# Kernel tuning notes

Measured on AMD Instinct MI355X. Metric: run time of the kernel, lower is better.

Reference implementation:

```python
import jax, jax.numpy as jnp
import numpy as np

B, S, E, H = 2, 2048, 1024, 16
D = E // H  # head dim = 64


def setup_inputs() -> dict:
    key = jax.random.key(0)
    ks = jax.random.split(key, 8)
    s = 1.0 / np.sqrt(E)  # keep projections well-scaled
    return {
        "query": jax.random.normal(ks[0], (B, S, E), jnp.float32),
        "key": jax.random.normal(ks[1], (B, S, E), jnp.float32),
        "value": jax.random.normal(ks[2], (B, S, E), jnp.float32),
        "Wq": jax.random.normal(ks[3], (E, E), jnp.float32) * s,
        "bq": jnp.zeros((E,), jnp.float32),
        "Wk": jax.random.normal(ks[4], (E, E), jnp.float32) * s,
        "bk": jnp.zeros((E,), jnp.float32),
        "Wv": jax.random.normal(ks[5], (E, E), jnp.float32) * s,
        "bv": jnp.zeros((E,), jnp.float32),
        "Wo": jax.random.normal(ks[6], (E, E), jnp.float32) * s,
        "bo": jnp.zeros((E,), jnp.float32),
    }


def _split_heads(x):
    # (b, s, h*d) -> (b, h, s, d)
    b, s, _ = x.shape
    return x.reshape(b, s, H, D).transpose(0, 2, 1, 3)


def reference(query, key, value, Wq, bq, Wk, bk, Wv, bv, Wo, bo):
    # Linear projections (torch Linear: x @ W^T + b)
    q = _split_heads(query @ Wq.T + bq)  # (b, h, s_q, d)
    k = _split_heads(key @ Wk.T + bk)    # (b, h, s_k, d)
    v = _split_heads(value @ Wv.T + bv)  # (b, h, s_k, d)
    # scaled dot-product attention; scale uses head dim of key
    scores = jnp.einsum("bhqd,bhkd->bhqk", q, k) * (D ** -0.5)
    attn = jax.nn.softmax(scores, axis=-1)  # (b, h, s_q, s_k)
    ctx = jnp.einsum("bhqk,bhkd->bhqd", attn, v)
    # merge heads: (b, h, s, d) -> (b, s, h*d)
    ctx = ctx.transpose(0, 2, 1, 3).reshape(B, S, H * D)
    out = ctx @ Wo.T + bo  # (b, s, out_dim)
    return out, attn
```

## Files before the change

kernel.cpp:

```cpp
#include <hip/hip_runtime.h>

typedef _Float16 f16;
typedef _Float16 f16x4 __attribute__((ext_vector_type(4)));
typedef _Float16 f16x8 __attribute__((ext_vector_type(8)));
typedef float f32x4 __attribute__((ext_vector_type(4)));

#define S_LEN 2048
#define EMB 1024
#define NH 16
#define HD 64
#define BATCH 2

__device__ __forceinline__ void gload_lds16(const void* g, void* l) {
  __builtin_amdgcn_global_load_lds(
      (const __attribute__((address_space(1))) void*)g,
      (__attribute__((address_space(3))) void*)l, 16, 0, 0);
}

__global__ __launch_bounds__(256) void cast_kernel(const float* __restrict__ in,
                                                   f16* __restrict__ out, int n4) {
  int i = blockIdx.x * 256 + threadIdx.x;
  if (i >= n4) return;
  const float4 v = reinterpret_cast<const float4*>(in)[i];
  f16x4 o;
  o[0] = (f16)v.x; o[1] = (f16)v.y; o[2] = (f16)v.z; o[3] = (f16)v.w;
  reinterpret_cast<f16x4*>(out)[i] = o;
}

template <int MODE>
__global__ __launch_bounds__(256) void gemm_bt(const f16* __restrict__ A,
                                               const f16* __restrict__ Bw,
                                               const float* __restrict__ bias,
                                               void* __restrict__ outp,
                                               int M, int N, int K) {
  __shared__ f16 As[128 * 64];
  __shared__ f16 Bs[64 * 64];
  const int tid = threadIdx.x;
  const int w = tid >> 6, lane = tid & 63;
  const int lg = lane >> 4, l15 = lane & 15;
  const int m0 = blockIdx.y * 128, n0 = blockIdx.x * 64;
  f32x4 acc[2][4] = {};
  for (int k0 = 0; k0 < K; k0 += 64) {
#pragma unroll
    for (int i = 0; i < 4; i++) {
      int c = i * 4 + w, o = c * 64 + lane;
      gload_lds16(A + (size_t)(m0 + (o >> 3)) * K + k0 + ((o & 7) << 3), As + c * 512);
    }
#pragma unroll
    for (int i = 0; i < 2; i++) {
      int c = i * 4 + w, o = c * 64 + lane;
      gload_lds16(Bw + (size_t)(n0 + (o >> 3)) * K + k0 + ((o & 7) << 3), Bs + c * 512);
    }
    __syncthreads();
#pragma unroll
    for (int kk = 0; kk < 2; kk++) {
      f16x8 af[2], bf[4];
#pragma unroll
      for (int mi = 0; mi < 2; mi++)
        af[mi] = *(const f16x8*)&As[(w * 32 + mi * 16 + l15) * 64 + kk * 32 + lg * 8];
#pragma unroll
      for (int ni = 0; ni < 4; ni++)
        bf[ni] = *(const f16x8*)&Bs[(ni * 16 + l15) * 64 + kk * 32 + lg * 8];
#pragma unroll
      for (int mi = 0; mi < 2; mi++)
#pragma unroll
        for (int ni = 0; ni < 4; ni++)
          acc[mi][ni] =
              __builtin_amdgcn_mfma_f32_16x16x32_f16(af[mi], bf[ni], acc[mi][ni], 0, 0, 0);
    }
    __syncthreads();
  }
#pragma unroll
  for (int mi = 0; mi < 2; mi++)
#pragma unroll
    for (int ni = 0; ni < 4; ni++) {
      const int gn = n0 + ni * 16 + l15;
      const float bv = bias[gn];
#pragma unroll
      for (int r = 0; r < 4; r++) {
        const int gm = m0 + w * 32 + mi * 16 + lg * 4 + r;
        const float v = acc[mi][ni][r] + bv;
        if (MODE == 1) {
          ((float*)outp)[(size_t)gm * N + gn] = v;
        } else {
          const int b = gm >> 11, s = gm & 2047;
          const int h = gn >> 6, d = gn & 63;
          ((f16*)outp)[(((size_t)(b * NH + h)) * S_LEN + s) * HD + d] = (f16)v;
        }
      }
    }
}

__global__ __launch_bounds__(256) void attn_kernel(const f16* __restrict__ Qp,
                                                   const f16* __restrict__ Kp,
                                                   const f16* __restrict__ Vp,
                                                   float* __restrict__ attn_out,
                                                   f16* __restrict__ ctx_out) {
  __shared__ f16 Vt[64 * 136];
  __shared__ f16 Ps[4][16 * 136];
  const int tid = threadIdx.x;
  const int w = tid >> 6, lane = tid & 63;
  const int lg = lane >> 4, l15 = lane & 15;
  const int bh = blockIdx.y;
  const int b = bh >> 4, h = bh & 15;
  const int q0 = blockIdx.x * 64;
  const f16* Qbh = Qp + (size_t)bh * S_LEN * HD;
  const f16* Kbh = Kp + (size_t)bh * S_LEN * HD;
  const f16* Vbh = Vp + (size_t)bh * S_LEN * HD;
  const int qrow_base = q0 + w * 16;

  f16x8 qf[2];
#pragma unroll
  for (int kk = 0; kk < 2; kk++)
    qf[kk] = *(const f16x8*)&Qbh[(size_t)(qrow_base + l15) * HD + kk * 32 + lg * 8];

  float m[4], l[4];
#pragma unroll
  for (int r = 0; r < 4; r++) { m[r] = -1e30f; l[r] = 0.f; }

  for (int kt = 0; kt < S_LEN; kt += 128) {
    f32x4 sf[8] = {};
#pragma unroll
    for (int kk = 0; kk < 2; kk++)
#pragma unroll
      for (int nf = 0; nf < 8; nf++) {
        f16x8 kf = *(const f16x8*)&Kbh[(size_t)(kt + nf * 16 + l15) * HD + kk * 32 + lg * 8];
        sf[nf] = __builtin_amdgcn_mfma_f32_16x16x32_f16(qf[kk], kf, sf[nf], 0, 0, 0);
      }
#pragma unroll
    for (int r = 0; r < 4; r++) {
      float pm = sf[0][r];
#pragma unroll
      for (int nf = 1; nf < 8; nf++) pm = fmaxf(pm, sf[nf][r]);
      pm *= 0.125f;
#pragma unroll
      for (int ofs = 1; ofs < 16; ofs <<= 1) pm = fmaxf(pm, __shfl_xor(pm, ofs));
      const float mn = fmaxf(m[r], pm);
      float ps = 0.f;
#pragma unroll
      for (int nf = 0; nf < 8; nf++) ps += __expf(sf[nf][r] * 0.125f - mn);
#pragma unroll
      for (int ofs = 1; ofs < 16; ofs <<= 1) ps += __shfl_xor(ps, ofs);
      l[r] = l[r] * __expf(m[r] - mn) + ps;
      m[r] = mn;
    }
  }
  float invl[4];
#pragma unroll
  for (int r = 0; r < 4; r++) invl[r] = 1.0f / l[r];

  f32x4 cacc[4] = {};
  for (int kt = 0; kt < S_LEN; kt += 128) {
#pragma unroll
    for (int i = 0; i < 4; i++) {
      int ch = i * 256 + tid;
      int ky = ch >> 3, d0 = (ch & 7) << 3;
      f16x8 v = *(const f16x8*)&Vbh[(size_t)(kt + ky) * HD + d0];
#pragma unroll
      for (int j = 0; j < 8; j++) Vt[(d0 + j) * 136 + ky] = v[j];
    }
    __syncthreads();

    f32x4 sf[8] = {};
#pragma unroll
    for (int kk = 0; kk < 2; kk++)
#pragma unroll
      for (int nf = 0; nf < 8; nf++) {
        f16x8 kf = *(const f16x8*)&Kbh[(size_t)(kt + nf * 16 + l15) * HD + kk * 32 + lg * 8];
        sf[nf] = __builtin_amdgcn_mfma_f32_16x16x32_f16(qf[kk], kf, sf[nf], 0, 0, 0);
      }
#pragma unroll
    for (int nf = 0; nf < 8; nf++)
#pragma unroll
      for (int r = 0; r < 4; r++) {
        const float p = __expf(sf[nf][r] * 0.125f - m[r]) * invl[r];
        const int qrow = qrow_base + lg * 4 + r;
        attn_out[((size_t)bh * S_LEN + qrow) * S_LEN + kt + nf * 16 + l15] = p;
        Ps[w][(lg * 4 + r) * 136 + nf * 16 + l15] = (f16)p;
      }
#pragma unroll
    for (int kk2 = 0; kk2 < 4; kk2++) {
      f16x8 pf = *(const f16x8*)&Ps[w][l15 * 136 + kk2 * 32 + lg * 8];
#pragma unroll
      for (int nf2 = 0; nf2 < 4; nf2++) {
        f16x8 vf = *(const f16x8*)&Vt[(nf2 * 16 + l15) * 136 + kk2 * 32 + lg * 8];
        cacc[nf2] = __builtin_amdgcn_mfma_f32_16x16x32_f16(pf, vf, cacc[nf2], 0, 0, 0);
      }
    }
    __syncthreads();
  }
#pragma unroll
  for (int nf2 = 0; nf2 < 4; nf2++)
#pragma unroll
    for (int r = 0; r < 4; r++) {
      const int qrow = qrow_base + lg * 4 + r;
      const int gr = b * S_LEN + qrow;
      const int gc = h * HD + nf2 * 16 + l15;
      ctx_out[(size_t)gr * EMB + gc] = (f16)cacc[nf2][r];
    }
}

extern "C" void kernel_launch(void* const* d_in, const int* in_sizes, int n_in,
                              void* d_out, int out_size, void* d_ws, size_t ws_size,
                              hipStream_t stream) {
  const float* query = (const float*)d_in[0];
  const float* key_i = (const float*)d_in[1];
  const float* value = (const float*)d_in[2];
  const float* Wq = (const float*)d_in[3];
  const float* bq = (const float*)d_in[4];
  const float* Wk = (const float*)d_in[5];
  const float* bk = (const float*)d_in[6];
  const float* Wv = (const float*)d_in[7];
  const float* bv = (const float*)d_in[8];
  const float* Wo = (const float*)d_in[9];
  const float* bo = (const float*)d_in[10];

  float* out = (float*)d_out;
  float* attn = out + (size_t)BATCH * S_LEN * EMB;

  f16* ws = (f16*)d_ws;
  const size_t NTOK = (size_t)BATCH * S_LEN;
  f16* Qh = ws;
  f16* Kh = Qh + NTOK * EMB;
  f16* Vh = Kh + NTOK * EMB;
  f16* Wqh = Vh + NTOK * EMB;
  f16* Wkh = Wqh + (size_t)EMB * EMB;
  f16* Wvh = Wkh + (size_t)EMB * EMB;
  f16* Woh = Wvh + (size_t)EMB * EMB;
  f16* Qp = Woh + (size_t)EMB * EMB;
  f16* Kp = Qp + NTOK * EMB;
  f16* Vp = Kp + NTOK * EMB;
  f16* ctx = Vp + NTOK * EMB;

  const int n4_x = (int)(NTOK * EMB / 4);
  const int n4_w = (int)((size_t)EMB * EMB / 4);
  cast_kernel<<<n4_x / 256, 256, 0, stream>>>(query, Qh, n4_x);
  cast_kernel<<<n4_x / 256, 256, 0, stream>>>(key_i, Kh, n4_x);
  cast_kernel<<<n4_x / 256, 256, 0, stream>>>(value, Vh, n4_x);
  cast_kernel<<<n4_w / 256, 256, 0, stream>>>(Wq, Wqh, n4_w);
  cast_kernel<<<n4_w / 256, 256, 0, stream>>>(Wk, Wkh, n4_w);
  cast_kernel<<<n4_w / 256, 256, 0, stream>>>(Wv, Wvh, n4_w);
  cast_kernel<<<n4_w / 256, 256, 0, stream>>>(Wo, Woh, n4_w);

  dim3 ggrid(EMB / 64, (unsigned)(NTOK / 128));
  gemm_bt<0><<<ggrid, 256, 0, stream>>>(Qh, Wqh, bq, Qp, (int)NTOK, EMB, EMB);
  gemm_bt<0><<<ggrid, 256, 0, stream>>>(Kh, Wkh, bk, Kp, (int)NTOK, EMB, EMB);
  gemm_bt<0><<<ggrid, 256, 0, stream>>>(Vh, Wvh, bv, Vp, (int)NTOK, EMB, EMB);

  attn_kernel<<<dim3(S_LEN / 64, BATCH * NH), 256, 0, stream>>>(Qp, Kp, Vp, attn, ctx);

  gemm_bt<1><<<ggrid, 256, 0, stream>>>(ctx, Woh, bo, out, (int)NTOK, EMB, EMB);
}
```

Before: 1.085 ms.

## Pre-transpose V in projection epilogue, swizzle LDS, prefetch V tiles, use exp2 softmax

The V projection GEMM now writes V transposed per head (d-major), so the attention kernel can copy V tiles into LDS with 16-byte vector stores into an XOR-swizzled layout instead of scattering scalar transposes. The next V tile is loaded into registers while the current tile is computed, with barriers arranged around a single LDS buffer. Softmax is rewritten in base 2 with the scale folded into Q in fp16 and the normalizer folded into the max via log2, which removes per-element multiplies. The risks are slightly different rounding from pre-scaling Q in fp16, and strided scalar stores in the V GEMM epilogue.

```diff
diff --git a/kernel.cpp b/kernel.cpp
--- a/kernel.cpp
+++ b/kernel.cpp
@@ -85,7 +85,10 @@
         } else {
           const int b = gm >> 11, s = gm & 2047;
           const int h = gn >> 6, d = gn & 63;
-          ((f16*)outp)[(((size_t)(b * NH + h)) * S_LEN + s) * HD + d] = (f16)v;
+          if (MODE == 0)
+            ((f16*)outp)[(((size_t)(b * NH + h)) * S_LEN + s) * HD + d] = (f16)v;
+          else
+            ((f16*)outp)[(((size_t)(b * NH + h)) * HD + d) * S_LEN + s] = (f16)v;
         }
       }
     }
@@ -93,10 +96,10 @@
 
 __global__ __launch_bounds__(256) void attn_kernel(const f16* __restrict__ Qp,
                                                    const f16* __restrict__ Kp,
-                                                   const f16* __restrict__ Vp,
+                                                   const f16* __restrict__ VtG,
                                                    float* __restrict__ attn_out,
                                                    f16* __restrict__ ctx_out) {
-  __shared__ f16 Vt[64 * 136];
+  __shared__ f16 Vt[64 * 128];
   __shared__ f16 Ps[4][16 * 136];
   const int tid = threadIdx.x;
   const int w = tid >> 6, lane = tid & 63;
@@ -106,17 +109,21 @@
   const int q0 = blockIdx.x * 64;
   const f16* Qbh = Qp + (size_t)bh * S_LEN * HD;
   const f16* Kbh = Kp + (size_t)bh * S_LEN * HD;
-  const f16* Vbh = Vp + (size_t)bh * S_LEN * HD;
+  const f16* Vtbh = VtG + (size_t)bh * HD * S_LEN;
   const int qrow_base = q0 + w * 16;
 
   f16x8 qf[2];
-#pragma unroll
-  for (int kk = 0; kk < 2; kk++)
+  const f16 qsc = (f16)0.18033688f;
+#pragma unroll
+  for (int kk = 0; kk < 2; kk++) {
     qf[kk] = *(const f16x8*)&Qbh[(size_t)(qrow_base + l15) * HD + kk * 32 + lg * 8];
-
-  float m[4], l[4];
-#pragma unroll
-  for (int r = 0; r < 4; r++) { m[r] = -1e30f; l[r] = 0.f; }
+#pragma unroll
+    for (int j = 0; j < 8; j++) qf[kk][j] *= qsc;
+  }
+
+  float m2[4], l[4];
+#pragma unroll
+  for (int r = 0; r < 4; r++) { m2[r] = -1e30f; l[r] = 0.f; }
 
   for (int kt = 0; kt < S_LEN; kt += 128) {
     f32x4 sf[8] = {};
@@ -132,34 +139,47 @@
       float pm = sf[0][r];
 #pragma unroll
       for (int nf = 1; nf < 8; nf++) pm = fmaxf(pm, sf[nf][r]);
-      pm *= 0.125f;
 #pragma unroll
       for (int ofs = 1; ofs < 16; ofs <<= 1) pm = fmaxf(pm, __shfl_xor(pm, ofs));
-      const float mn = fmaxf(m[r], pm);
+      const float mn = fmaxf(m2[r], pm);
       float ps = 0.f;
 #pragma unroll
-      for (int nf = 0; nf < 8; nf++) ps += __expf(sf[nf][r] * 0.125f - mn);
+      for (int nf = 0; nf < 8; nf++) ps += exp2f(sf[nf][r] - mn);
 #pragma unroll
       for (int ofs = 1; ofs < 16; ofs <<= 1) ps += __shfl_xor(ps, ofs);
-      l[r] = l[r] * __expf(m[r] - mn) + ps;
-      m[r] = mn;
-    }
-  }
-  float invl[4];
-#pragma unroll
-  for (int r = 0; r < 4; r++) invl[r] = 1.0f / l[r];
+      l[r] = l[r] * exp2f(m2[r] - mn) + ps;
+      m2[r] = mn;
+    }
+  }
+#pragma unroll
+  for (int r = 0; r < 4; r++) m2[r] += log2f(l[r]);
+
+#define STAGE_LOAD(KT)                                                      \
+  {                                                                         \
+    _Pragma("unroll") for (int c = 0; c < 4; c++) {                         \
+      const int idx = c * 256 + tid;                                        \
+      const int rr = idx >> 4, bb = idx & 15;                               \
+      vreg[c] = *(const f16x8*)&Vtbh[(size_t)rr * S_LEN + (KT) + bb * 8];   \
+    }                                                                       \
+  }
+#define STAGE_WRITE()                                                       \
+  {                                                                         \
+    _Pragma("unroll") for (int c = 0; c < 4; c++) {                         \
+      const int idx = c * 256 + tid;                                        \
+      const int rr = idx >> 4, bb = idx & 15;                               \
+      *(f16x8*)((char*)Vt + rr * 256 + ((bb ^ (rr & 7)) << 4)) = vreg[c];   \
+    }                                                                       \
+  }
 
   f32x4 cacc[4] = {};
-  for (int kt = 0; kt < S_LEN; kt += 128) {
-#pragma unroll
-    for (int i = 0; i < 4; i++) {
-      int ch = i * 256 + tid;
-      int ky = ch >> 3, d0 = (ch & 7) << 3;
-      f16x8 v = *(const f16x8*)&Vbh[(size_t)(kt + ky) * HD + d0];
-#pragma unroll
-      for (int j = 0; j < 8; j++) Vt[(d0 + j) * 136 + ky] = v[j];
-    }
-    __syncthreads();
+  f16x8 vreg[4];
+  STAGE_LOAD(0);
+  STAGE_WRITE();
+  asm volatile("s_waitcnt lgkmcnt(0)\n\ts_barrier" ::: "memory");
+
+  for (int t = 0; t < 16; t++) {
+    const int kt = t * 128;
+    STAGE_LOAD(((t + 1) & 15) * 128);
 
     f32x4 sf[8] = {};
 #pragma unroll
@@ -173,7 +193,7 @@
     for (int nf = 0; nf < 8; nf++)
 #pragma unroll
       for (int r = 0; r < 4; r++) {
-        const float p = __expf(sf[nf][r] * 0.125f - m[r]) * invl[r];
+        const float p = exp2f(sf[nf][r] - m2[r]);
         const int qrow = qrow_base + lg * 4 + r;
         attn_out[((size_t)bh * S_LEN + qrow) * S_LEN + kt + nf * 16 + l15] = p;
         Ps[w][(lg * 4 + r) * 136 + nf * 16 + l15] = (f16)p;
@@ -183,11 +203,14 @@
       f16x8 pf = *(const f16x8*)&Ps[w][l15 * 136 + kk2 * 32 + lg * 8];
 #pragma unroll
       for (int nf2 = 0; nf2 < 4; nf2++) {
-        f16x8 vf = *(const f16x8*)&Vt[(nf2 * 16 + l15) * 136 + kk2 * 32 + lg * 8];
+        const int rr = nf2 * 16 + l15, bb = kk2 * 4 + lg;
+        f16x8 vf = *(const f16x8*)((const char*)Vt + rr * 256 + ((bb ^ (rr & 7)) << 4));
         cacc[nf2] = __builtin_amdgcn_mfma_f32_16x16x32_f16(pf, vf, cacc[nf2], 0, 0, 0);
       }
     }
-    __syncthreads();
+    asm volatile("s_barrier" ::: "memory");
+    STAGE_WRITE();
+    asm volatile("s_waitcnt lgkmcnt(0)\n\ts_barrier" ::: "memory");
   }
 #pragma unroll
   for (int nf2 = 0; nf2 < 4; nf2++)
@@ -198,6 +221,8 @@
       const int gc = h * HD + nf2 * 16 + l15;
       ctx_out[(size_t)gr * EMB + gc] = (f16)cacc[nf2][r];
     }
+#undef STAGE_LOAD
+#undef STAGE_WRITE
 }
 
 extern "C" void kernel_launch(void* const* d_in, const int* in_sizes, int n_in,
@@ -229,8 +254,8 @@
   f16* Woh = Wvh + (size_t)EMB * EMB;
   f16* Qp = Woh + (size_t)EMB * EMB;
   f16* Kp = Qp + NTOK * EMB;
-  f16* Vp = Kp + NTOK * EMB;
-  f16* ctx = Vp + NTOK * EMB;
+  f16* VtG = Kp + NTOK * EMB;
+  f16* ctx = VtG + NTOK * EMB;
 
   const int n4_x = (int)(NTOK * EMB / 4);
   const int n4_w = (int)((size_t)EMB * EMB / 4);
@@ -245,9 +270,9 @@
   dim3 ggrid(EMB / 64, (unsigned)(NTOK / 128));
   gemm_bt<0><<<ggrid, 256, 0, stream>>>(Qh, Wqh, bq, Qp, (int)NTOK, EMB, EMB);
   gemm_bt<0><<<ggrid, 256, 0, stream>>>(Kh, Wkh, bk, Kp, (int)NTOK, EMB, EMB);
-  gemm_bt<0><<<ggrid, 256, 0, stream>>>(Vh, Wvh, bv, Vp, (int)NTOK, EMB, EMB);
-
-  attn_kernel<<<dim3(S_LEN / 64, BATCH * NH), 256, 0, stream>>>(Qp, Kp, Vp, attn, ctx);
+  gemm_bt<2><<<ggrid, 256, 0, stream>>>(Vh, Wvh, bv, VtG, (int)NTOK, EMB, EMB);
+
+  attn_kernel<<<dim3(S_LEN / 64, BATCH * NH), 256, 0, stream>>>(Qp, Kp, VtG, attn, ctx);
 
   gemm_bt<1><<<ggrid, 256, 0, stream>>>(ctx, Woh, bo, out, (int)NTOK, EMB, EMB);
 }
```

After: 970.1 us. -10.6%, faster.
